# Optimization experiments

Measured on AMD Instinct MI355X. Metric: run time of the kernel, lower is better.

The kernel has to match this reference:

```python
import jax, jax.numpy as jnp
import numpy as np

N, D, K = 500_000, 64, 512


def setup_inputs() -> dict:
    key = jax.random.key(0)
    kx, kc = jax.random.split(key)
    x = jax.random.normal(kx, (N, D), dtype=jnp.float32)
    centroids = jax.random.normal(kc, (K, D), dtype=jnp.float32)
    return {"x": x, "centroids": centroids}


def reference(x, centroids):
    x2 = jnp.sum(x * x, axis=1, keepdims=True)            # [N, 1]
    c2 = jnp.sum(centroids * centroids, axis=1)           # [K]
    d2 = x2 + c2[None, :] - 2.0 * jnp.einsum('nd,kd->nk', x, centroids)
    d2 = jnp.maximum(d2, 0.0)
    # sqrt is monotonic so argmin over d2 == argmin over cdist
    label = jnp.argmin(d2, axis=1)                        # [N] int
    return label
```

## Files before the change

kernel.cpp:

```cpp
#include <hip/hip_runtime.h>

#define DIM 64
#define KC 512
#define BLK 256
#define PT 4
#define CG 128
#define NT (CG / 16)
#define MARGIN 1e-3f
#define LIST_CAP 500000

typedef _Float16 half8   __attribute__((ext_vector_type(8)));
typedef float    floatx4 __attribute__((ext_vector_type(4)));

__device__ __forceinline__ void async_cp16(_Float16* lds_base, const _Float16* g_lane) {
    __builtin_amdgcn_global_load_lds(
        (const __attribute__((address_space(1))) unsigned int*)(g_lane),
        (__attribute__((address_space(3))) unsigned int*)(lds_base),
        16, 0, 0);
}

__global__ __launch_bounds__(BLK) void kmeans_prep(
    const float* __restrict__ c, _Float16* __restrict__ frH,
    _Float16* __restrict__ frL, float* __restrict__ g_sc2,
    unsigned* __restrict__ rs_count)
{
    const int b = blockIdx.x;
    if (b < 128) {
        const int e  = b * BLK + threadIdx.x;
        const int cr = e >> 6, d = e & 63;
        const int T  = cr >> 4, ni = cr & 15;
        const int ch = d >> 5, q = (d >> 3) & 3, j = d & 7;
        const int pos = ((T * 2 + ch) * 64 + (q * 16 + ni)) * 8 + j;
        const float f = c[e];
        const _Float16 h = (_Float16)f;
        frH[pos] = h;
        frL[pos] = (_Float16)((f - (float)h) * 2048.0f);
    } else {
        if (b == 128 && threadIdx.x == 0) *rs_count = 0u;
        const int k = (b - 128) * BLK + threadIdx.x;
        const float* crow = c + (long)k * DIM;
        float s0 = 0.f, s1 = 0.f, s2 = 0.f, s3 = 0.f;
        #pragma unroll
        for (int d = 0; d < DIM; d += 4) {
            s0 = fmaf(crow[d + 0], crow[d + 0], s0);
            s1 = fmaf(crow[d + 1], crow[d + 1], s1);
            s2 = fmaf(crow[d + 2], crow[d + 2], s2);
            s3 = fmaf(crow[d + 3], crow[d + 3], s3);
        }
        g_sc2[k] = (s0 + s1) + (s2 + s3);
    }
}

__global__ __launch_bounds__(BLK)
__attribute__((amdgpu_waves_per_eu(2)))
void kmeans_mfma(const float* __restrict__ x,
                 const _Float16* __restrict__ frH, const _Float16* __restrict__ frL,
                 const float* __restrict__ g_sc2, int* __restrict__ out,
                 unsigned* __restrict__ rs_count, int* __restrict__ rs_list, int n)
{
    __shared__ _Float16 shH[NT * 2 * 64 * 8];
    __shared__ _Float16 shL[NT * 2 * 64 * 8];
    __shared__ float    s_sc2[KC];

    const int tid  = threadIdx.x;
    const int wave = tid >> 6;
    const int lane = tid & 63;
    const int nidx = lane & 15;
    const int quad = lane >> 4;

    const long jobBase = ((long)blockIdx.x * 4 + wave) * 64;

    half8 ah[PT][2], al[PT][2];
    #pragma unroll
    for (int pt = 0; pt < PT; ++pt) {
        long row = jobBase + pt * 16 + nidx;
        if (row > (long)n - 1) row = (long)n - 1;
        #pragma unroll
        for (int ch = 0; ch < 2; ++ch) {
            const float* xp = x + row * DIM + ch * 32 + quad * 8;
            float4 v0 = *(const float4*)xp;
            float4 v1 = *(const float4*)(xp + 4);
            float fs[8] = {v0.x, v0.y, v0.z, v0.w, v1.x, v1.y, v1.z, v1.w};
            #pragma unroll
            for (int j = 0; j < 8; ++j) {
                _Float16 h = (_Float16)fs[j];
                ah[pt][ch][j] = h;
                al[pt][ch][j] = (_Float16)((fs[j] - (float)h) * 2048.0f);
            }
        }
    }

    float best[PT][4], sec[PT][4];
    int   bidx[PT][4];
    #pragma unroll
    for (int pt = 0; pt < PT; ++pt)
        #pragma unroll
        for (int r = 0; r < 4; ++r) {
            best[pt][r] = 3.402823466e38f;
            sec[pt][r]  = 3.402823466e38f;
            bidx[pt][r] = 0;
        }

    for (int g = 0; g < 4; ++g) {
        if (g) __syncthreads();

        {
            const _Float16* srcH = frH + (long)g * (NT * 2 * 64 * 8);
            const _Float16* srcL = frL + (long)g * (NT * 2 * 64 * 8);
            #pragma unroll
            for (int ii = 0; ii < 4; ++ii) {
                const int chunk = wave * 256 + ii * 64;
                async_cp16(shH + (long)chunk * 8, srcH + (long)(chunk + lane) * 8);
                async_cp16(shL + (long)chunk * 8, srcL + (long)(chunk + lane) * 8);
            }
        }
        if (g == 0) {
            for (int k2 = tid; k2 < KC; k2 += BLK) s_sc2[k2] = g_sc2[k2];
        }
        __syncthreads();

        #pragma unroll 2
        for (int t = 0; t < NT; ++t) {
            const half8 bh0 = *(const half8*)&shH[((t * 2 + 0) * 64 + lane) * 8];
            const half8 bh1 = *(const half8*)&shH[((t * 2 + 1) * 64 + lane) * 8];
            const half8 bl0 = *(const half8*)&shL[((t * 2 + 0) * 64 + lane) * 8];
            const half8 bl1 = *(const half8*)&shL[((t * 2 + 1) * 64 + lane) * 8];
            const float cc2 = s_sc2[g * CG + t * 16 + nidx];
            const int  kidx = g * CG + t * 16 + nidx;
            #pragma unroll
            for (int pt = 0; pt < PT; ++pt) {
                floatx4 am = {0.f, 0.f, 0.f, 0.f};
                floatx4 ac = {0.f, 0.f, 0.f, 0.f};
                am = __builtin_amdgcn_mfma_f32_16x16x32_f16(ah[pt][0], bh0, am, 0, 0, 0);
                am = __builtin_amdgcn_mfma_f32_16x16x32_f16(ah[pt][1], bh1, am, 0, 0, 0);
                ac = __builtin_amdgcn_mfma_f32_16x16x32_f16(ah[pt][0], bl0, ac, 0, 0, 0);
                ac = __builtin_amdgcn_mfma_f32_16x16x32_f16(ah[pt][1], bl1, ac, 0, 0, 0);
                ac = __builtin_amdgcn_mfma_f32_16x16x32_f16(al[pt][0], bh0, ac, 0, 0, 0);
                ac = __builtin_amdgcn_mfma_f32_16x16x32_f16(al[pt][1], bh1, ac, 0, 0, 0);
                #pragma unroll
                for (int r = 0; r < 4; ++r) {
                    const float dot = fmaf(ac[r], 4.8828125e-4f, am[r]);
                    const float v   = fmaf(-2.0f, dot, cc2);
                    const bool lt = v < best[pt][r];
                    sec[pt][r]  = fminf(sec[pt][r], lt ? best[pt][r] : v);
                    best[pt][r] = lt ? v : best[pt][r];
                    bidx[pt][r] = lt ? kidx : bidx[pt][r];
                }
            }
        }
    }

    #pragma unroll
    for (int off = 1; off < 16; off <<= 1) {
        #pragma unroll
        for (int pt = 0; pt < PT; ++pt)
            #pragma unroll
            for (int r = 0; r < 4; ++r) {
                const float ob = __shfl_xor(best[pt][r], off, 64);
                const int   oi = __shfl_xor(bidx[pt][r], off, 64);
                const float os = __shfl_xor(sec[pt][r],  off, 64);
                const bool lt = (ob < best[pt][r]) ||
                                (ob == best[pt][r] && oi < bidx[pt][r]);
                const float loser = lt ? best[pt][r] : ob;
                sec[pt][r]  = fminf(fminf(sec[pt][r], os), loser);
                best[pt][r] = lt ? ob : best[pt][r];
                bidx[pt][r] = lt ? oi : bidx[pt][r];
            }
    }

    const int pt_w = nidx >> 2;
    const int r_w  = lane & 3;
    float b = 0.f, s = 0.f; int bi = 0;
    #pragma unroll
    for (int pt = 0; pt < PT; ++pt)
        #pragma unroll
        for (int r = 0; r < 4; ++r) {
            const bool m = (pt == pt_w) && (r == r_w);
            b  = m ? best[pt][r] : b;
            s  = m ? sec[pt][r]  : s;
            bi = m ? bidx[pt][r] : bi;
        }
    const long p = jobBase + (long)pt_w * 16 + quad * 4 + r_w;

    if (p < n) {
        out[p] = bi;
        if (!(s - b > MARGIN)) {
            const unsigned idx = atomicAdd(rs_count, 1u);
            if (idx < LIST_CAP) rs_list[idx] = (int)p;
        }
    }
}

__global__ __launch_bounds__(BLK) void kmeans_rescan(
    const float* __restrict__ x, const float* __restrict__ c,
    const float* __restrict__ g_sc2, const unsigned* __restrict__ rs_count,
    const int* __restrict__ rs_list, int* __restrict__ out)
{
    const int lane  = threadIdx.x & 63;
    const int gwave = (blockIdx.x * BLK + threadIdx.x) >> 6;
    const int nwave = gridDim.x * (BLK / 64);
    unsigned cnt = *rs_count;
    if (cnt > LIST_CAP) cnt = LIST_CAP;

    for (unsigned j = gwave; j < cnt; j += nwave) {
        const int p = rs_list[j];
        const float* xrow = x + (long)p * DIM;

        float x20 = 0.f, x21 = 0.f, x22 = 0.f, x23 = 0.f;
        #pragma unroll
        for (int d = 0; d < DIM; d += 4) {
            x20 = fmaf(xrow[d + 0], xrow[d + 0], x20);
            x21 = fmaf(xrow[d + 1], xrow[d + 1], x21);
            x22 = fmaf(xrow[d + 2], xrow[d + 2], x22);
            x23 = fmaf(xrow[d + 3], xrow[d + 3], x23);
        }
        const float x2 = (x20 + x21) + (x22 + x23);

        float bb = 3.402823466e38f; int bbi = 0x7fffffff;
        #pragma unroll
        for (int kk = 0; kk < 8; ++kk) {
            const int k = lane * 8 + kk;
            const float* crow = c + (long)k * DIM;
            float d0 = 0.f, d1 = 0.f, d2a = 0.f, d3 = 0.f;
            #pragma unroll
            for (int d = 0; d < DIM; d += 4) {
                d0  = fmaf(crow[d + 0], xrow[d + 0], d0);
                d1  = fmaf(crow[d + 1], xrow[d + 1], d1);
                d2a = fmaf(crow[d + 2], xrow[d + 2], d2a);
                d3  = fmaf(crow[d + 3], xrow[d + 3], d3);
            }
            const float dot = (d0 + d1) + (d2a + d3);
            float d2v = (x2 + g_sc2[k]) - 2.0f * dot;
            d2v = fmaxf(d2v, 0.0f);
            const bool l2 = d2v < bb;
            bb  = l2 ? d2v : bb;
            bbi = l2 ? k   : bbi;
        }
        #pragma unroll
        for (int off = 1; off < 64; off <<= 1) {
            const float ob = __shfl_xor(bb, off, 64);
            const int   oi = __shfl_xor(bbi, off, 64);
            const bool take = (ob < bb) || (ob == bb && oi < bbi);
            bb  = take ? ob : bb;
            bbi = take ? oi : bbi;
        }
        if (lane == 0) out[p] = bbi;
    }
}

extern "C" void kernel_launch(void* const* d_in, const int* in_sizes, int n_in,
                              void* d_out, int out_size, void* d_ws, size_t ws_size,
                              hipStream_t stream) {
    const float* x = (const float*)d_in[0];
    const float* c = (const float*)d_in[1];
    int* out = (int*)d_out;
    const int n = in_sizes[0] / DIM;

    _Float16* frH   = (_Float16*)d_ws;
    _Float16* frL   = frH + (KC * DIM);
    float*    gsc2  = (float*)(frL + (KC * DIM));
    unsigned* cnt   = (unsigned*)(gsc2 + KC);
    int*      rlist = (int*)(cnt + 4);

    kmeans_prep<<<130, BLK, 0, stream>>>(c, frH, frL, gsc2, cnt);

    const int jobs   = (n + 63) / 64;
    const int blocks = (jobs + 3) / 4;
    kmeans_mfma<<<blocks, BLK, 0, stream>>>(x, frH, frL, gsc2, out, cnt, rlist, n);

    kmeans_rescan<<<512, BLK, 0, stream>>>(x, c, gsc2, cnt, rlist, out);
}
```

Before: 335.3 us.

## Use 512-thread blocks with larger centroid tiles and fold norms into MFMA accumulators

Doubles the block to 8 waves and the centroid group to 256, so each LDS-staged fragment tile serves twice as many rows and the kernel runs two group iterations instead of four. It also seeds the MFMA accumulator with -0.5*||c||^2 and tracks a maximum of dot minus half-norm. That drops the per-element scale-and-subtract, and the scaled accumulate is vectorised. The ambiguity margin is rescaled, slightly wider than an exact halving, and the rescan grid is shrunk to 128 blocks. The cost is higher LDS use per block (about 64KB) and possibly more points sent to the rescan path.

Measured after the change: 352.8 us. 5.2% more time.

```diff
diff --git a/kernel.cpp b/kernel.cpp
--- a/kernel.cpp
+++ b/kernel.cpp
@@ -2,11 +2,12 @@
 
 #define DIM 64
 #define KC 512
-#define BLK 256
+#define BLKM 512
+#define BLKP 256
 #define PT 4
-#define CG 128
+#define CG 256
 #define NT (CG / 16)
-#define MARGIN 1e-3f
+#define MARGINH 7.5e-4f
 #define LIST_CAP 500000
 
 typedef _Float16 half8   __attribute__((ext_vector_type(8)));
@@ -19,14 +20,14 @@
         16, 0, 0);
 }
 
-__global__ __launch_bounds__(BLK) void kmeans_prep(
+__global__ __launch_bounds__(BLKP) void kmeans_prep(
     const float* __restrict__ c, _Float16* __restrict__ frH,
     _Float16* __restrict__ frL, float* __restrict__ g_sc2,
     unsigned* __restrict__ rs_count)
 {
     const int b = blockIdx.x;
     if (b < 128) {
-        const int e  = b * BLK + threadIdx.x;
+        const int e  = b * BLKP + threadIdx.x;
         const int cr = e >> 6, d = e & 63;
         const int T  = cr >> 4, ni = cr & 15;
         const int ch = d >> 5, q = (d >> 3) & 3, j = d & 7;
@@ -37,7 +38,7 @@
         frL[pos] = (_Float16)((f - (float)h) * 2048.0f);
     } else {
         if (b == 128 && threadIdx.x == 0) *rs_count = 0u;
-        const int k = (b - 128) * BLK + threadIdx.x;
+        const int k = (b - 128) * BLKP + threadIdx.x;
         const float* crow = c + (long)k * DIM;
         float s0 = 0.f, s1 = 0.f, s2 = 0.f, s3 = 0.f;
         #pragma unroll
@@ -51,7 +52,7 @@
     }
 }
 
-__global__ __launch_bounds__(BLK)
+__global__ __launch_bounds__(BLKM)
 __attribute__((amdgpu_waves_per_eu(2)))
 void kmeans_mfma(const float* __restrict__ x,
                  const _Float16* __restrict__ frH, const _Float16* __restrict__ frL,
@@ -68,7 +69,7 @@
     const int nidx = lane & 15;
     const int quad = lane >> 4;
 
-    const long jobBase = ((long)blockIdx.x * 4 + wave) * 64;
+    const long jobBase = ((long)blockIdx.x * 8 + wave) * 64;
 
     half8 ah[PT][2], al[PT][2];
     #pragma unroll
@@ -96,12 +97,12 @@
     for (int pt = 0; pt < PT; ++pt)
         #pragma unroll
         for (int r = 0; r < 4; ++r) {
-            best[pt][r] = 3.402823466e38f;
-            sec[pt][r]  = 3.402823466e38f;
+            best[pt][r] = -3.402823466e38f;
+            sec[pt][r]  = -3.402823466e38f;
             bidx[pt][r] = 0;
         }
 
-    for (int g = 0; g < 4; ++g) {
+    for (int g = 0; g < 2; ++g) {
         if (g) __syncthreads();
 
         {
@@ -115,7 +116,7 @@
             }
         }
         if (g == 0) {
-            for (int k2 = tid; k2 < KC; k2 += BLK) s_sc2[k2] = g_sc2[k2];
+            for (int k2 = tid; k2 < KC; k2 += BLKM) s_sc2[k2] = g_sc2[k2];
         }
         __syncthreads();
 
@@ -125,11 +126,11 @@
             const half8 bh1 = *(const half8*)&shH[((t * 2 + 1) * 64 + lane) * 8];
             const half8 bl0 = *(const half8*)&shL[((t * 2 + 0) * 64 + lane) * 8];
             const half8 bl1 = *(const half8*)&shL[((t * 2 + 1) * 64 + lane) * 8];
-            const float cc2 = s_sc2[g * CG + t * 16 + nidx];
-            const int  kidx = g * CG + t * 16 + nidx;
+            const float negh = -0.5f * s_sc2[g * CG + t * 16 + nidx];
+            const int   kidx = g * CG + t * 16 + nidx;
             #pragma unroll
             for (int pt = 0; pt < PT; ++pt) {
-                floatx4 am = {0.f, 0.f, 0.f, 0.f};
+                floatx4 am = {negh, negh, negh, negh};
                 floatx4 ac = {0.f, 0.f, 0.f, 0.f};
                 am = __builtin_amdgcn_mfma_f32_16x16x32_f16(ah[pt][0], bh0, am, 0, 0, 0);
                 am = __builtin_amdgcn_mfma_f32_16x16x32_f16(ah[pt][1], bh1, am, 0, 0, 0);
@@ -137,14 +138,13 @@
                 ac = __builtin_amdgcn_mfma_f32_16x16x32_f16(ah[pt][1], bl1, ac, 0, 0, 0);
                 ac = __builtin_amdgcn_mfma_f32_16x16x32_f16(al[pt][0], bh0, ac, 0, 0, 0);
                 ac = __builtin_amdgcn_mfma_f32_16x16x32_f16(al[pt][1], bh1, ac, 0, 0, 0);
+                const floatx4 vv = am + ac * 4.8828125e-4f;
                 #pragma unroll
                 for (int r = 0; r < 4; ++r) {
-                    const float dot = fmaf(ac[r], 4.8828125e-4f, am[r]);
-                    const float v   = fmaf(-2.0f, dot, cc2);
-                    const bool lt = v < best[pt][r];
-                    sec[pt][r]  = fminf(sec[pt][r], lt ? best[pt][r] : v);
-                    best[pt][r] = lt ? v : best[pt][r];
-                    bidx[pt][r] = lt ? kidx : bidx[pt][r];
+                    const bool gt = vv[r] > best[pt][r];
+                    sec[pt][r]  = fmaxf(sec[pt][r], gt ? best[pt][r] : vv[r]);
+                    best[pt][r] = gt ? vv[r] : best[pt][r];
+                    bidx[pt][r] = gt ? kidx  : bidx[pt][r];
                 }
             }
         }
@@ -159,12 +159,12 @@
                 const float ob = __shfl_xor(best[pt][r], off, 64);
                 const int   oi = __shfl_xor(bidx[pt][r], off, 64);
                 const float os = __shfl_xor(sec[pt][r],  off, 64);
-                const bool lt = (ob < best[pt][r]) ||
-                                (ob == best[pt][r] && oi < bidx[pt][r]);
-                const float loser = lt ? best[pt][r] : ob;
-                sec[pt][r]  = fminf(fminf(sec[pt][r], os), loser);
-                best[pt][r] = lt ? ob : best[pt][r];
-                bidx[pt][r] = lt ? oi : bidx[pt][r];
+                const bool take = (ob > best[pt][r]) ||
+                                  (ob == best[pt][r] && oi < bidx[pt][r]);
+                const float loser = take ? best[pt][r] : ob;
+                sec[pt][r]  = fmaxf(fmaxf(sec[pt][r], os), loser);
+                best[pt][r] = take ? ob : best[pt][r];
+                bidx[pt][r] = take ? oi : bidx[pt][r];
             }
     }
 
@@ -184,21 +184,21 @@
 
     if (p < n) {
         out[p] = bi;
-        if (!(s - b > MARGIN)) {
+        if (!(b - s > MARGINH)) {
             const unsigned idx = atomicAdd(rs_count, 1u);
             if (idx < LIST_CAP) rs_list[idx] = (int)p;
         }
     }
 }
 
-__global__ __launch_bounds__(BLK) void kmeans_rescan(
+__global__ __launch_bounds__(BLKP) void kmeans_rescan(
     const float* __restrict__ x, const float* __restrict__ c,
     const float* __restrict__ g_sc2, const unsigned* __restrict__ rs_count,
     const int* __restrict__ rs_list, int* __restrict__ out)
 {
     const int lane  = threadIdx.x & 63;
-    const int gwave = (blockIdx.x * BLK + threadIdx.x) >> 6;
-    const int nwave = gridDim.x * (BLK / 64);
+    const int gwave = (blockIdx.x * BLKP + threadIdx.x) >> 6;
+    const int nwave = gridDim.x * (BLKP / 64);
     unsigned cnt = *rs_count;
     if (cnt > LIST_CAP) cnt = LIST_CAP;
 
@@ -262,11 +262,11 @@
     unsigned* cnt   = (unsigned*)(gsc2 + KC);
     int*      rlist = (int*)(cnt + 4);
 
-    kmeans_prep<<<130, BLK, 0, stream>>>(c, frH, frL, gsc2, cnt);
+    kmeans_prep<<<130, BLKP, 0, stream>>>(c, frH, frL, gsc2, cnt);
 
     const int jobs   = (n + 63) / 64;
-    const int blocks = (jobs + 3) / 4;
-    kmeans_mfma<<<blocks, BLK, 0, stream>>>(x, frH, frL, gsc2, out, cnt, rlist, n);
-
-    kmeans_rescan<<<512, BLK, 0, stream>>>(x, c, gsc2, cnt, rlist, out);
-}
+    const int blocks = (jobs + 7) / 8;
+    kmeans_mfma<<<blocks, BLKM, 0, stream>>>(x, frH, frL, gsc2, out, cnt, rlist, n);
+
+    kmeans_rescan<<<128, BLKP, 0, stream>>>(x, c, gsc2, cnt, rlist, out);
+}
```
